# Performance work log

Hardware: AMD Instinct MI355X
Metric: run time of the kernel (lower is better)

Reference implementation:

```python
import jax, jax.numpy as jnp
import numpy as np

EMBED_DIM = 768
NUM_HEADS = 12
PROJ_DIM = EMBED_DIM // NUM_HEADS  # 64
M_FEATURES = 128
EPS = 1e-6


def _orthogonal_projection(key, m, d):
    # Faithful to create_projection_matrix(scaling=0): stacked transposed Q-factors
    # of iid gaussian blocks, rescaled by chi-distributed row norms.
    nb_full_blocks = m // d
    keys = jax.random.split(key, nb_full_blocks + 2)
    blocks = []
    for i in range(nb_full_blocks):
        q, _ = jnp.linalg.qr(jax.random.normal(keys[i], (d, d)))
        blocks.append(q.T)
    rem = m - nb_full_blocks * d
    if rem > 0:
        q, _ = jnp.linalg.qr(jax.random.normal(keys[nb_full_blocks], (d, d)))
        blocks.append(q.T[:rem])
    final = jnp.vstack(blocks)
    multiplier = jnp.linalg.norm(jax.random.normal(keys[-1], (m, d)), axis=1)
    return multiplier[:, None] * final


def setup_inputs() -> dict:
    key = jax.random.key(0)
    ks = jax.random.split(key, 8)
    B, L, E = 4, 4096, EMBED_DIM
    s = 1.0 / np.sqrt(E)
    inp = {
        "x": jax.random.normal(ks[0], (B, L, E), jnp.float32),
        "Wq": jax.random.normal(ks[1], (E, E), jnp.float32) * s,
        "bq": jnp.zeros((E,), jnp.float32),
        "Wk": jax.random.normal(ks[2], (E, E), jnp.float32) * s,
        "bk": jnp.zeros((E,), jnp.float32),
        "Wv": jax.random.normal(ks[3], (E, E), jnp.float32) * s,
        "bv": jnp.zeros((E,), jnp.float32),
        "Wo": jax.random.normal(ks[4], (E, E), jnp.float32) * s,
        "bo": jnp.zeros((E,), jnp.float32),
        "proj": _orthogonal_projection(ks[5], M_FEATURES, PROJ_DIM),
    }
    return inp


def _softmax_kernel(data, projection_matrix):
    # data: [B, L, H, D]; projection_matrix: [M, D]
    data_normalizer = 1.0 / jnp.sqrt(jnp.sqrt(jnp.float32(PROJ_DIM)))
    data = data_normalizer * data
    ratio = 1.0 / jnp.sqrt(jnp.float32(projection_matrix.shape[0]))
    data_dash = jnp.einsum("blhd,md->blhm", data, projection_matrix)
    diag_data = jnp.sum(jnp.square(data), axis=-1, keepdims=True) / 2.0  # [B,L,H,1]
    stab = jnp.max(data_dash, axis=-1, keepdims=True)
    return ratio * (jnp.exp(data_dash - diag_data - stab) + EPS)


def reference(x, Wq, bq, Wk, bk, Wv, bv, Wo, bo, proj):
    B, L, E = x.shape
    H, D = NUM_HEADS, PROJ_DIM

    def split_heads(t):
        return t.reshape(B, L, H, D)

    q = split_heads(x @ Wq + bq)
    k = split_heads(x @ Wk + bk)
    v = split_heads(x @ Wv + bv)

    q_prime = _softmax_kernel(q, proj)  # [B,L,H,M]
    k_prime = _softmax_kernel(k, proj)  # [B,L,H,M]

    # Linear-attention numerator/denominator (O(L) in sequence length).
    kvs = jnp.einsum("blhm,blhd->bhmd", k_prime, v)          # [B,H,M,D]
    num = jnp.einsum("blhm,bhmd->blhd", q_prime, kvs)        # [B,L,H,D]
    ks_sum = jnp.sum(k_prime, axis=1)                         # [B,H,M]
    den = jnp.einsum("blhm,bhm->blh", q_prime, ks_sum)        # [B,L,H]
    attention = num / den[..., None]                          # [B,L,H,D]

    # Faithful to source: transpose to [B,H,L,D] then reshape to [B,-1,E].
    concat = jnp.transpose(attention, (0, 2, 1, 3)).reshape(B, -1, E)
    return concat @ Wo + bo
```

## Files before the change

### kernel.cpp

```cpp
#include <hip/hip_runtime.h>

typedef _Float16 f16;
typedef __attribute__((ext_vector_type(8))) _Float16 half8;
typedef __attribute__((ext_vector_type(4))) _Float16 half4;
typedef __attribute__((ext_vector_type(4))) float f32x4;

#define DEVINL static __device__ __forceinline__

constexpr float NORMALIZER = 0.35355339059327373f;
constexpr float RATIO      = 0.08838834764831845f;
constexpr float FEPS       = 1e-6f;

constexpr size_t OFF_WQKVT = 0;
constexpr size_t OFF_WOT   = OFF_WQKVT + (size_t)2304*768*2;
constexpr size_t OFF_PROJF = OFF_WOT   + (size_t)768*768*2;
constexpr size_t OFF_KS    = OFF_PROJF + (size_t)128*64*2;
constexpr size_t OFF_KSP   = OFF_KS    + (size_t)48*128*4;
constexpr size_t OFF_KVST  = OFF_KSP   + (size_t)48*64*128*4;
constexpr size_t OFF_KVSP  = OFF_KVST  + (size_t)48*64*128*2;
constexpr size_t OFF_X16   = OFF_KVSP  + (size_t)16*48*128*64*4;
constexpr size_t OFF_ATT   = OFF_X16;
constexpr size_t OFF_Q16   = OFF_X16 + (size_t)16384*768*2;
constexpr size_t OFF_K16   = OFF_Q16 + (size_t)16384*768*2;
constexpr size_t OFF_VT    = OFF_K16 + (size_t)16384*768*2;
constexpr size_t OFF_KPT   = OFF_VT  + (size_t)16384*768*2;

DEVINL void gload_lds16(const f16* g, f16* lds) {
  __builtin_amdgcn_global_load_lds(
      (const __attribute__((address_space(1))) void*)g,
      (__attribute__((address_space(3))) void*)lds, 16, 0, 0);
}

#define VMCNT0    asm volatile("s_waitcnt vmcnt(0)" ::: "memory")
#define BAR       __builtin_amdgcn_s_barrier()

DEVINL void gemm256c(const f16* __restrict__ Ag, const f16* __restrict__ Bg,
                     f16* smem, f32x4 (&acc)[8][3], int w, int lane)
{
  constexpr int NT = 24;
  const int wm = w >> 2, wn = w & 3;
  const int c = lane & 15, g16 = lane >> 4;
  const int tid = threadIdx.x;

#pragma unroll
  for (int i = 0; i < 8; ++i)
#pragma unroll
    for (int j = 0; j < 3; ++j)
      acc[i][j] = f32x4{0.f, 0.f, 0.f, 0.f};

  auto SA = [&](int tt, f16* buf) {
#pragma unroll
    for (int u = 0; u < 2; ++u) {
      const int id = u * 512 + tid;
      const int r = id >> 2, sg = id & 3;
      const int seg = sg ^ ((r >> 1) & 3);
      gload_lds16(Ag + (size_t)r * 768 + tt * 32 + seg * 8, buf + (u * 512 + w * 64) * 8);
    }
  };
  auto SB = [&](int tt, f16* buf) {
    {
      const int r = tid >> 2, sg = tid & 3;
      const int seg = sg ^ ((r >> 1) & 3);
      gload_lds16(Bg + (size_t)r * 768 + tt * 32 + seg * 8, buf + 8192 + w * 64 * 8);
    }
    if (w < 4) {
      const int id = 512 + tid;
      const int r = id >> 2, sg = id & 3;
      const int seg = sg ^ ((r >> 1) & 3);
      gload_lds16(Bg + (size_t)r * 768 + tt * 32 + seg * 8, buf + 8192 + (512 + w * 64) * 8);
    }
  };
  auto RDA = [&](const f16* buf, int mh, half8 (&av)[4]) {
#pragma unroll
    for (int i = 0; i < 4; ++i) {
      const int r = wm * 128 + mh * 64 + i * 16 + c;
      av[i] = *(const half8*)(buf + r * 32 + ((g16 ^ ((r >> 1) & 3)) << 3));
    }
  };
  auto RDB = [&](const f16* buf, half8 (&bv)[3]) {
#pragma unroll
    for (int j = 0; j < 3; ++j) {
      const int r = wn * 48 + j * 16 + c;
      bv[j] = *(const half8*)(buf + 8192 + r * 32 + ((g16 ^ ((r >> 1) & 3)) << 3));
    }
  };

  SA(0, smem); SB(0, smem);
  VMCNT0;
  BAR;

#pragma unroll 1
  for (int t = 0; t < NT; ++t) {
    f16* bufR = smem + (t & 1) * 14336;
    f16* bufW = smem + ((t & 1) ^ 1) * 14336;
    const bool st = (t + 1) < NT;
    half8 av[4], bv[3];

    RDA(bufR, 0, av); RDB(bufR, bv);
    if (st) SA(t + 1, bufW);
    __builtin_amdgcn_s_setprio(1);
#pragma unroll
    for (int i = 0; i < 4; ++i)
#pragma unroll
      for (int j = 0; j < 3; ++j)
        acc[i][j] = __builtin_amdgcn_mfma_f32_16x16x32_f16(av[i], bv[j], acc[i][j], 0, 0, 0);
    __builtin_amdgcn_s_setprio(0);
    RDA(bufR, 1, av);
    if (st) SB(t + 1, bufW);
    __builtin_amdgcn_s_setprio(1);
#pragma unroll
    for (int i = 0; i < 4; ++i)
#pragma unroll
      for (int j = 0; j < 3; ++j)
        acc[4 + i][j] = __builtin_amdgcn_mfma_f32_16x16x32_f16(av[i], bv[j], acc[4 + i][j], 0, 0, 0);
    __builtin_amdgcn_s_setprio(0);
    VMCNT0;
    BAR;
  }
}

__global__ __launch_bounds__(512, 2) void k_gemm_qkv8(const f16* __restrict__ X16, const f16* __restrict__ WT,
    const float* __restrict__ bq, const float* __restrict__ bk, const float* __restrict__ bv,
    f16* __restrict__ Qo, f16* __restrict__ Ko, f16* __restrict__ VT)
{
  __shared__ f16 smem[28672];
  f32x4 acc[8][3];
  const int lin = blockIdx.x;
  const int xcd = lin & 7, chunk = lin >> 3;
  const int bx = xcd * 8 + chunk / 12;
  const int by = chunk % 12;
  const int brow0 = bx * 256;
  const int t = threadIdx.x, w = t >> 6, lane = t & 63;
  gemm256c(X16 + (size_t)brow0 * 768, WT + (size_t)by * 192 * 768, smem, acc, w, lane);

  const int wm = w >> 2, wn = w & 3;
  const int c = lane & 15, g16 = lane >> 4;
  const int which = by >> 2;
  const int colhdr = (by & 3) * 192;
  const float* bias = which == 0 ? bq : (which == 1 ? bk : bv);
  float bb[3];
#pragma unroll
  for (int j = 0; j < 3; ++j) bb[j] = bias[colhdr + wn * 48 + j * 16 + c];

  f16* ep = smem;
  if (which < 2) {
    f16* QK = which == 0 ? Qo : Ko;
#pragma unroll 1
    for (int p = 0; p < 2; ++p) {
      __syncthreads();
      if (wm == p) {
#pragma unroll
        for (int ii = 0; ii < 8; ++ii)
#pragma unroll
          for (int j = 0; j < 3; ++j)
#pragma unroll
            for (int r = 0; r < 4; ++r)
              ep[((ii >> 2) * 64 + (ii & 3) * 16 + g16 * 4 + r) * 200 + wn * 48 + j * 16 + c]
                  = (f16)(acc[ii][j][r] + bb[j]);
      }
      __syncthreads();
      const int row = t >> 2, sg = (t & 3) * 48;
      f16* dst = QK + (size_t)(brow0 + p * 128 + row) * 768 + colhdr + sg;
      const f16* sp = ep + row * 200 + sg;
#pragma unroll
      for (int u = 0; u < 6; ++u) *(half8*)(dst + u * 8) = *(const half8*)(sp + u * 8);
    }
  } else {
    const int bIdx = brow0 >> 12;
#pragma unroll 1
    for (int p = 0; p < 2; ++p) {
      __syncthreads();
      if (wm == p) {
#pragma unroll
        for (int ii = 0; ii < 8; ++ii)
#pragma unroll
          for (int j = 0; j < 3; ++j)
#pragma unroll
            for (int r = 0; r < 4; ++r)
              ep[(wn * 48 + j * 16 + c) * 136 + (ii >> 2) * 64 + (ii & 3) * 16 + g16 * 4 + r]
                  = (f16)(acc[ii][j][r] + bb[j]);
      }
      __syncthreads();
      if (t < 384) {
        const int cl = t >> 1, sg = (t & 1) * 64;
        const int vcol = colhdr + cl;
        const int h = vcol >> 6, d = vcol & 63;
        f16* dst = VT + ((size_t)(bIdx * 12 + h) * 64 + d) * 4096 + (brow0 & 4095) + p * 128 + sg;
        const f16* sp = ep + cl * 136 + sg;
#pragma unroll
        for (int u = 0; u < 8; ++u) *(half8*)(dst + u * 8) = *(const half8*)(sp + u * 8);
      }
    }
  }
}

__global__ __launch_bounds__(512, 2) void k_gemm_out8(const f16* __restrict__ ATT, const f16* __restrict__ WOT,
    const float* __restrict__ bo, float* __restrict__ out)
{
  __shared__ f16 smem[28672];
  f32x4 acc[8][3];
  const int lin = blockIdx.x;
  const int xcd = lin & 7, chunk = lin >> 3;
  const int bx = xcd * 8 + (chunk >> 2);
  const int by = chunk & 3;
  const int brow0 = bx * 256;
  const int t = threadIdx.x, w = t >> 6, lane = t & 63;
  gemm256c(ATT + (size_t)brow0 * 768, WOT + (size_t)by * 192 * 768, smem, acc, w, lane);

  const int wm = w >> 2, wn = w & 3;
  const int c = lane & 15, g16 = lane >> 4;
  float bb[3];
#pragma unroll
  for (int j = 0; j < 3; ++j) bb[j] = bo[by * 192 + wn * 48 + j * 16 + c];
#pragma unroll
  for (int ii = 0; ii < 8; ++ii) {
    const int row0 = brow0 + wm * 128 + (ii >> 2) * 64 + (ii & 3) * 16 + g16 * 4;
#pragma unroll
    for (int j = 0; j < 3; ++j) {
      const int col = by * 192 + wn * 48 + j * 16 + c;
#pragma unroll
      for (int r = 0; r < 4; ++r)
        out[(size_t)(row0 + r) * 768 + col] = acc[ii][j][r] + bb[j];
    }
  }
}

template<int BN>
DEVINL void gemm_tile(const f16* A, int lda, const f16* Bt, int ldb, int K,
                      f16* As, f16* Bs, f32x4 (&acc)[4][BN/32])
{
  constexpr int NF = BN/32;
  const int t = threadIdx.x;
  const int w = t >> 6, lane = t & 63;
  const int g = lane >> 4, c = lane & 15;
  const int wr = w >> 1, wc = w & 1;
  const int srow = lane >> 2;
  const int sseg = (lane & 3) * 8;

#pragma unroll
  for (int i = 0; i < 4; ++i)
#pragma unroll
    for (int j = 0; j < NF; ++j)
      acc[i][j] = f32x4{0.f, 0.f, 0.f, 0.f};

  for (int k0 = 0; k0 < K; k0 += 32) {
#pragma unroll
    for (int r = 0; r < 2; ++r) {
      const int rowblk = (w + 4*r) * 16;
      gload_lds16(A + (size_t)(rowblk + srow) * lda + k0 + sseg, As + rowblk*32);
    }
#pragma unroll
    for (int r = 0; r < BN/64; ++r) {
      const int rowblk = (w + 4*r) * 16;
      gload_lds16(Bt + (size_t)(rowblk + srow) * ldb + k0 + sseg, Bs + rowblk*32);
    }
    __syncthreads();
    half8 av[4], bv[NF];
#pragma unroll
    for (int i = 0; i < 4; ++i)
      av[i] = *(const half8*)(As + (wr*64 + i*16 + c)*32 + g*8);
#pragma unroll
    for (int j = 0; j < NF; ++j)
      bv[j] = *(const half8*)(Bs + (wc*(BN/2) + j*16 + c)*32 + g*8);
#pragma unroll
    for (int i = 0; i < 4; ++i)
#pragma unroll
      for (int j = 0; j < NF; ++j)
        acc[i][j] = __builtin_amdgcn_mfma_f32_16x16x32_f16(av[i], bv[j], acc[i][j], 0, 0, 0);
    __syncthreads();
  }
}

__global__ __launch_bounds__(256) void k_cast_x(const float* __restrict__ X, f16* __restrict__ X16)
{
  const size_t i = ((size_t)blockIdx.x*256 + threadIdx.x) * 4;
  const float4 v = *(const float4*)(X + i);
  half4 h;
  h[0] = (f16)v.x; h[1] = (f16)v.y; h[2] = (f16)v.z; h[3] = (f16)v.w;
  *(half4*)(X16 + i) = h;
}

__global__ __launch_bounds__(256) void k_transpose_w4(const float* __restrict__ Wq, const float* __restrict__ Wk,
    const float* __restrict__ Wv, const float* __restrict__ Wo, f16* __restrict__ WQKVT, f16* __restrict__ WOT)
{
  __shared__ float ls[64][65];
  const int t = threadIdx.x;
  const int k0 = blockIdx.x*64, n0 = blockIdx.y*64, z = blockIdx.z;
  const float* W = z == 0 ? Wq : (z == 1 ? Wk : (z == 2 ? Wv : Wo));
  f16* Wt = z < 3 ? (WQKVT + (size_t)z*768*768) : WOT;
#pragma unroll
  for (int it = 0; it < 4; ++it) {
    const int r = it*16 + (t >> 4);
    const int cs = (t & 15) * 4;
    const float4 v = *(const float4*)(W + (size_t)(k0 + r)*768 + n0 + cs);
    ls[r][cs+0] = v.x; ls[r][cs+1] = v.y; ls[r][cs+2] = v.z; ls[r][cs+3] = v.w;
  }
  __syncthreads();
  const int n = t >> 2;
  const int seg = (t & 3) * 16;
  half8 ov[2];
#pragma unroll
  for (int i = 0; i < 16; ++i) ov[i>>3][i&7] = (f16)ls[seg + i][n];
  f16* dst = Wt + (size_t)(n0 + n)*768 + k0 + seg;
  *(half8*)dst = ov[0];
  *(half8*)(dst + 8) = ov[1];
}

__global__ __launch_bounds__(256) void k_cast_proj(const float* __restrict__ P, f16* __restrict__ PF)
{
  const int i = blockIdx.x*256 + threadIdx.x;
  PF[i] = (f16)(NORMALIZER * P[i]);
}

DEVINL void feat_common(const f16* base, const f16* PROJF,
                        f16* qs, f16* ps, float* dd, float* diag_s)
{
  const int t = threadIdx.x, w = t >> 6, lane = t & 63;
#pragma unroll
  for (int it = 0; it < 2; ++it) {
    const int rowblk = it*32 + w*8;
    gload_lds16(base + (size_t)(rowblk + (lane>>3))*768 + (lane&7)*8, qs + rowblk*64);
  }
#pragma unroll
  for (int it = 0; it < 4; ++it) {
    const int rowblk = it*32 + w*8;
    gload_lds16(PROJF + (size_t)(rowblk + (lane>>3))*64 + (lane&7)*8, ps + rowblk*64);
  }
  __syncthreads();
  if (t < 64) {
    float s = 0.f;
    for (int d = 0; d < 64; ++d) { const float qv = (float)qs[t*64 + d]; s += qv*qv; }
    diag_s[t] = 0.0625f * s;
  }
  const int g = lane >> 4, c = lane & 15;
  const int wr = w >> 1, wc = w & 1;
  f32x4 facc[2][4];
#pragma unroll
  for (int i = 0; i < 2; ++i)
#pragma unroll
    for (int j = 0; j < 4; ++j) facc[i][j] = f32x4{0.f,0.f,0.f,0.f};
#pragma unroll
  for (int kk = 0; kk < 2; ++kk) {
    half8 av[2], bv[4];
#pragma unroll
    for (int i = 0; i < 2; ++i) av[i] = *(const half8*)(qs + (wr*32 + i*16 + c)*64 + kk*32 + g*8);
#pragma unroll
    for (int j = 0; j < 4; ++j) bv[j] = *(const half8*)(ps + (wc*64 + j*16 + c)*64 + kk*32 + g*8);
#pragma unroll
    for (int i = 0; i < 2; ++i)
#pragma unroll
      for (int j = 0; j < 4; ++j)
        facc[i][j] = __builtin_amdgcn_mfma_f32_16x16x32_f16(av[i], bv[j], facc[i][j], 0, 0, 0);
  }
#pragma unroll
  for (int i = 0; i < 2; ++i)
#pragma unroll
    for (int j = 0; j < 4; ++j)
#pragma unroll
      for (int r = 0; r < 4; ++r)
        dd[(wr*32 + i*16 + g*4 + r)*129 + wc*64 + j*16 + c] = facc[i][j][r];
  __syncthreads();
}

__global__ __launch_bounds__(256) void k_kfeat(const f16* __restrict__ Kin, const f16* __restrict__ PROJF,
    f16* __restrict__ KPT, float* __restrict__ KSP)
{
  __shared__ f16 qs[64*64];
  __shared__ f16 ps[128*64];
  __shared__ float dd[64*129];
  __shared__ float diag_s[64];
  const int t = threadIdx.x;
  const int lb = blockIdx.x, bh = blockIdx.y;
  const int b = bh / 12, h = bh - b*12;
  feat_common(Kin + ((size_t)(b*4096 + lb*64))*768 + h*64, PROJF, qs, ps, dd, diag_s);
  const int l = t >> 2, s = t & 3;
  float v[32];
#pragma unroll
  for (int j = 0; j < 32; ++j) v[j] = dd[l*129 + s*32 + j];
  float mx = v[0];
#pragma unroll
  for (int j = 1; j < 32; ++j) mx = fmaxf(mx, v[j]);
  mx = fmaxf(mx, __shfl_xor(mx, 1));
  mx = fmaxf(mx, __shfl_xor(mx, 2));
  const float off = diag_s[l] + mx;
#pragma unroll
  for (int j = 0; j < 32; ++j) dd[l*129 + s*32 + j] = RATIO * (__expf(v[j] - off) + FEPS);
  __syncthreads();
  if (t < 128) {
    float sm = 0.f;
    for (int l2 = 0; l2 < 64; ++l2) sm += dd[l2*129 + t];
    KSP[((size_t)bh*64 + lb)*128 + t] = sm;
  }
  const int m = t >> 1, hf = t & 1;
  half8 ov[4];
#pragma unroll
  for (int i2 = 0; i2 < 32; ++i2) ov[i2>>3][i2&7] = (f16)dd[(hf*32 + i2)*129 + m];
  f16* dst = KPT + ((size_t)bh*128 + m)*4096 + lb*64 + hf*32;
#pragma unroll
  for (int q8 = 0; q8 < 4; ++q8) *(half8*)(dst + q8*8) = ov[q8];
}

__global__ __launch_bounds__(256) void k_kvs(const f16* __restrict__ KPT, const f16* __restrict__ VT,
    float* __restrict__ KVSP)
{
  __shared__ f16 As[128*32], Bs[64*32];
  f32x4 acc[4][2];
  const int chunk = blockIdx.x, bh = blockIdx.y;
  gemm_tile<64>(KPT + (size_t)bh*128*4096 + chunk*256, 4096,
                VT  + (size_t)bh*64*4096  + chunk*256, 4096, 256, As, Bs, acc);
  const int t = threadIdx.x, w = t>>6, lane = t&63, g = lane>>4, c = lane&15;
  const int wr = w>>1, wc = w&1;
  float* dst = KVSP + (size_t)(chunk*48 + bh)*128*64;
#pragma unroll
  for (int i = 0; i < 4; ++i) {
    const int row0 = wr*64 + i*16 + g*4;
#pragma unroll
    for (int j = 0; j < 2; ++j) {
      const int col = wc*32 + j*16 + c;
#pragma unroll
      for (int r = 0; r < 4; ++r) dst[(size_t)(row0 + r)*64 + col] = acc[i][j][r];
    }
  }
}

__global__ __launch_bounds__(256) void k_reduce(const float* __restrict__ KVSP, const float* __restrict__ KSP,
    f16* __restrict__ KVST, float* __restrict__ KS)
{
  const int i = blockIdx.x*256 + threadIdx.x;
  if (i < 48*128*64) {
    const int bh = i >> 13, md = i & 8191, m = md >> 6, d = md & 63;
    float s = 0.f;
#pragma unroll
    for (int c = 0; c < 16; ++c) s += KVSP[((size_t)(c*48 + bh)*128 + m)*64 + d];
    KVST[((size_t)bh*64 + d)*128 + m] = (f16)s;
  }
  if (i < 48*128) {
    const int bh = i >> 7, m = i & 127;
    float s = 0.f;
#pragma unroll 8
    for (int lb = 0; lb < 64; ++lb) s += KSP[((size_t)bh*64 + lb)*128 + m];
    KS[i] = s;
  }
}

__global__ __launch_bounds__(256) void k_qfn(const f16* __restrict__ Q, const f16* __restrict__ PROJF,
    const float* __restrict__ KS, const f16* __restrict__ KVST, f16* __restrict__ ATT)
{
  __shared__ f16 qs[64*64];
  __shared__ f16 ps[128*64];
  __shared__ float dd[64*129];
  __shared__ float diag_s[64];
  __shared__ float den_s[64];
  __shared__ f16 qp[64*128];
  __shared__ float ks_s[128];
  const int t = threadIdx.x;
  const int lb = blockIdx.x, bh = blockIdx.y;
  const int b = bh / 12, h = bh - b*12;
  if (t < 128) ks_s[t] = KS[bh*128 + t];
  feat_common(Q + ((size_t)(b*4096 + lb*64))*768 + h*64, PROJF, qs, ps, dd, diag_s);

  const int w = t >> 6, lane = t & 63, g16 = lane >> 4, c = lane & 15;
  const int wr = w >> 1, wc = w & 1;
  half8 bv2[2][4];
#pragma unroll
  for (int j = 0; j < 2; ++j) {
    const int d = wc*32 + j*16 + c;
#pragma unroll
    for (int kk = 0; kk < 4; ++kk)
      bv2[j][kk] = *(const half8*)(KVST + (size_t)bh*8192 + d*128 + kk*32 + g16*8);
  }

  const int l = t >> 2, s = t & 3;
  float v[32];
#pragma unroll
  for (int j = 0; j < 32; ++j) v[j] = dd[l*129 + s*32 + j];
  float mx = v[0];
#pragma unroll
  for (int j = 1; j < 32; ++j) mx = fmaxf(mx, v[j]);
  mx = fmaxf(mx, __shfl_xor(mx, 1));
  mx = fmaxf(mx, __shfl_xor(mx, 2));
  const float off = diag_s[l] + mx;
  half8 ov[4];
  float dp = 0.f;
#pragma unroll
  for (int j = 0; j < 32; ++j) {
    const float e = RATIO * (__expf(v[j] - off) + FEPS);
    ov[j>>3][j&7] = (f16)e;
    dp += e * ks_s[s*32 + j];
  }
  dp += __shfl_xor(dp, 1);
  dp += __shfl_xor(dp, 2);
  if (s == 0) den_s[l] = dp;
#pragma unroll
  for (int k = 0; k < 4; ++k)
    *(half8*)(qp + l*128 + (((4*s + k) ^ (l & 7)) << 3)) = ov[k];
  __syncthreads();

  f32x4 acc2[2][2];
#pragma unroll
  for (int i = 0; i < 2; ++i)
#pragma unroll
    for (int j = 0; j < 2; ++j) acc2[i][j] = f32x4{0.f,0.f,0.f,0.f};
#pragma unroll
  for (int kk = 0; kk < 4; ++kk) {
    half8 av2[2];
#pragma unroll
    for (int i = 0; i < 2; ++i) {
      const int l2 = wr*32 + i*16 + c;
      av2[i] = *(const half8*)(qp + l2*128 + (((kk*4 + g16) ^ (l2 & 7)) << 3));
    }
#pragma unroll
    for (int i = 0; i < 2; ++i)
#pragma unroll
      for (int j = 0; j < 2; ++j)
        acc2[i][j] = __builtin_amdgcn_mfma_f32_16x16x32_f16(av2[i], bv2[j][kk], acc2[i][j], 0, 0, 0);
  }

  f16* ep = ps;
#pragma unroll
  for (int i = 0; i < 2; ++i)
#pragma unroll
    for (int j = 0; j < 2; ++j)
#pragma unroll
      for (int r = 0; r < 4; ++r) {
        const int l3 = wr*32 + i*16 + g16*4 + r;
        ep[l3*72 + wc*32 + j*16 + c] = (f16)(acc2[i][j][r] / den_s[l3]);
      }
  __syncthreads();
  const int row = t >> 2, sg = (t & 3) * 16;
  f16* dst = ATT + ((size_t)bh*4096 + lb*64 + row)*64 + sg;
  const f16* sp = ep + row*72 + sg;
  *(half8*)dst = *(const half8*)sp;
  *(half8*)(dst + 8) = *(const half8*)(sp + 8);
}

extern "C" void kernel_launch(void* const* d_in, const int* in_sizes, int n_in,
                              void* d_out, int out_size, void* d_ws, size_t ws_size,
                              hipStream_t stream)
{
  const float* x    = (const float*)d_in[0];
  const float* Wq   = (const float*)d_in[1];
  const float* bq   = (const float*)d_in[2];
  const float* Wk   = (const float*)d_in[3];
  const float* bk   = (const float*)d_in[4];
  const float* Wv   = (const float*)d_in[5];
  const float* bv   = (const float*)d_in[6];
  const float* Wo   = (const float*)d_in[7];
  const float* bo   = (const float*)d_in[8];
  const float* proj = (const float*)d_in[9];
  float* out = (float*)d_out;
  char* ws = (char*)d_ws;

  f16*   WQKVT = (f16*)(ws + OFF_WQKVT);
  f16*   WOT   = (f16*)(ws + OFF_WOT);
  f16*   PROJF = (f16*)(ws + OFF_PROJF);
  float* KS    = (float*)(ws + OFF_KS);
  float* KSP   = (float*)(ws + OFF_KSP);
  f16*   KVST  = (f16*)(ws + OFF_KVST);
  float* KVSP  = (float*)(ws + OFF_KVSP);
  f16*   X16   = (f16*)(ws + OFF_X16);
  f16*   ATT   = (f16*)(ws + OFF_ATT);
  f16*   Q16   = (f16*)(ws + OFF_Q16);
  f16*   K16   = (f16*)(ws + OFF_K16);
  f16*   VT    = (f16*)(ws + OFF_VT);
  f16*   KPT   = (f16*)(ws + OFF_KPT);

  k_cast_x<<<12288, 256, 0, stream>>>(x, X16);
  k_transpose_w4<<<dim3(12,12,4), 256, 0, stream>>>(Wq, Wk, Wv, Wo, WQKVT, WOT);
  k_cast_proj<<<32, 256, 0, stream>>>(proj, PROJF);

  k_gemm_qkv8<<<768, 512, 0, stream>>>(X16, WQKVT, bq, bk, bv, Q16, K16, VT);
  k_kfeat<<<dim3(64,48), 256, 0, stream>>>(K16, PROJF, KPT, KSP);
  k_kvs<<<dim3(16,48), 256, 0, stream>>>(KPT, VT, KVSP);
  k_reduce<<<1536, 256, 0, stream>>>(KVSP, KSP, KVST, KS);
  k_qfn<<<dim3(64,48), 256, 0, stream>>>(Q16, PROJF, KS, KVST, ATT);
  k_gemm_out8<<<256, 512, 0, stream>>>(ATT, WOT, bo, out);
}
```

Measured before the change: 257.2 us.

## Fuse prep kernels, parallelize row reductions, and halve kvs split chunks

Merges the x cast, weight transposes and projection cast into one launch to cut launch overhead. In the feature kernels, the diagonal-norm and column-sum reductions are spread across all threads with shuffles instead of running on a subset with long serial loops. The kvs split-K count drops from 16 to 8 chunks, so each block does more work and the reduce step reads half as many partials. The trade-off is fewer blocks for kvs, which may leave the GPU underused.

```diff
diff --git a/kernel.cpp b/kernel.cpp
--- a/kernel.cpp
+++ b/kernel.cpp
@@ -18,7 +18,7 @@
 constexpr size_t OFF_KSP   = OFF_KS    + (size_t)48*128*4;
 constexpr size_t OFF_KVST  = OFF_KSP   + (size_t)48*64*128*4;
 constexpr size_t OFF_KVSP  = OFF_KVST  + (size_t)48*64*128*2;
-constexpr size_t OFF_X16   = OFF_KVSP  + (size_t)16*48*128*64*4;
+constexpr size_t OFF_X16   = OFF_KVSP  + (size_t)8*48*128*64*4;
 constexpr size_t OFF_ATT   = OFF_X16;
 constexpr size_t OFF_Q16   = OFF_X16 + (size_t)16384*768*2;
 constexpr size_t OFF_K16   = OFF_Q16 + (size_t)16384*768*2;
@@ -271,21 +271,27 @@
   }
 }
 
-__global__ __launch_bounds__(256) void k_cast_x(const float* __restrict__ X, f16* __restrict__ X16)
-{
-  const size_t i = ((size_t)blockIdx.x*256 + threadIdx.x) * 4;
-  const float4 v = *(const float4*)(X + i);
-  half4 h;
-  h[0] = (f16)v.x; h[1] = (f16)v.y; h[2] = (f16)v.z; h[3] = (f16)v.w;
-  *(half4*)(X16 + i) = h;
-}
-
-__global__ __launch_bounds__(256) void k_transpose_w4(const float* __restrict__ Wq, const float* __restrict__ Wk,
-    const float* __restrict__ Wv, const float* __restrict__ Wo, f16* __restrict__ WQKVT, f16* __restrict__ WOT)
+__global__ __launch_bounds__(256) void k_prep(const float* __restrict__ X, f16* __restrict__ X16,
+    const float* __restrict__ P, f16* __restrict__ PF,
+    const float* __restrict__ Wq, const float* __restrict__ Wk,
+    const float* __restrict__ Wv, const float* __restrict__ Wo,
+    f16* __restrict__ WQKVT, f16* __restrict__ WOT)
 {
   __shared__ float ls[64][65];
   const int t = threadIdx.x;
-  const int k0 = blockIdx.x*64, n0 = blockIdx.y*64, z = blockIdx.z;
+  if (blockIdx.x < 12288) {
+    const size_t i = ((size_t)blockIdx.x*256 + t) * 4;
+    const float4 v = *(const float4*)(X + i);
+    half4 h;
+    h[0] = (f16)v.x; h[1] = (f16)v.y; h[2] = (f16)v.z; h[3] = (f16)v.w;
+    *(half4*)(X16 + i) = h;
+    if (blockIdx.x == 0)
+      for (int i2 = t; i2 < 8192; i2 += 256) PF[i2] = (f16)(NORMALIZER * P[i2]);
+    return;
+  }
+  const int zz = blockIdx.x - 12288;
+  const int z = zz / 144, rem = zz - z*144;
+  const int k0 = (rem / 12) * 64, n0 = (rem % 12) * 64;
   const float* W = z == 0 ? Wq : (z == 1 ? Wk : (z == 2 ? Wv : Wo));
   f16* Wt = z < 3 ? (WQKVT + (size_t)z*768*768) : WOT;
 #pragma unroll
@@ -306,12 +312,6 @@
   *(half8*)(dst + 8) = ov[1];
 }
 
-__global__ __launch_bounds__(256) void k_cast_proj(const float* __restrict__ P, f16* __restrict__ PF)
-{
-  const int i = blockIdx.x*256 + threadIdx.x;
-  PF[i] = (f16)(NORMALIZER * P[i]);
-}
-
 DEVINL void feat_common(const f16* base, const f16* PROJF,
                         f16* qs, f16* ps, float* dd, float* diag_s)
 {
@@ -327,10 +327,19 @@
     gload_lds16(PROJF + (size_t)(rowblk + (lane>>3))*64 + (lane&7)*8, ps + rowblk*64);
   }
   __syncthreads();
-  if (t < 64) {
+  {
+    const int row = t >> 2, q = t & 3;
+    const f16* kr = qs + row*64 + q*16;
+    half8 v0 = *(const half8*)(kr);
+    half8 v1 = *(const half8*)(kr + 8);
     float s = 0.f;
-    for (int d = 0; d < 64; ++d) { const float qv = (float)qs[t*64 + d]; s += qv*qv; }
-    diag_s[t] = 0.0625f * s;
+#pragma unroll
+    for (int d2 = 0; d2 < 8; ++d2) { float a = (float)v0[d2]; s += a*a; }
+#pragma unroll
+    for (int d2 = 0; d2 < 8; ++d2) { float a = (float)v1[d2]; s += a*a; }
+    s += __shfl_xor(s, 1);
+    s += __shfl_xor(s, 2);
+    if (q == 0) diag_s[row] = 0.0625f * s;
   }
   const int g = lane >> 4, c = lane & 15;
   const int wr = w >> 1, wc = w & 1;
@@ -386,10 +395,13 @@
 #pragma unroll
   for (int j = 0; j < 32; ++j) dd[l*129 + s*32 + j] = RATIO * (__expf(v[j] - off) + FEPS);
   __syncthreads();
-  if (t < 128) {
+  {
+    const int m = t >> 1, hf = t & 1;
     float sm = 0.f;
-    for (int l2 = 0; l2 < 64; ++l2) sm += dd[l2*129 + t];
-    KSP[((size_t)bh*64 + lb)*128 + t] = sm;
+#pragma unroll 8
+    for (int l2 = hf*32; l2 < hf*32 + 32; ++l2) sm += dd[l2*129 + m];
+    sm += __shfl_xor(sm, 1);
+    if (hf == 0) KSP[((size_t)bh*64 + lb)*128 + m] = sm;
   }
   const int m = t >> 1, hf = t & 1;
   half8 ov[4];
@@ -406,8 +418,8 @@
   __shared__ f16 As[128*32], Bs[64*32];
   f32x4 acc[4][2];
   const int chunk = blockIdx.x, bh = blockIdx.y;
-  gemm_tile<64>(KPT + (size_t)bh*128*4096 + chunk*256, 4096,
-                VT  + (size_t)bh*64*4096  + chunk*256, 4096, 256, As, Bs, acc);
+  gemm_tile<64>(KPT + (size_t)bh*128*4096 + chunk*512, 4096,
+                VT  + (size_t)bh*64*4096  + chunk*512, 4096, 512, As, Bs, acc);
   const int t = threadIdx.x, w = t>>6, lane = t&63, g = lane>>4, c = lane&15;
   const int wr = w>>1, wc = w&1;
   float* dst = KVSP + (size_t)(chunk*48 + bh)*128*64;
@@ -431,7 +443,7 @@
     const int bh = i >> 13, md = i & 8191, m = md >> 6, d = md & 63;
     float s = 0.f;
 #pragma unroll
-    for (int c = 0; c < 16; ++c) s += KVSP[((size_t)(c*48 + bh)*128 + m)*64 + d];
+    for (int c = 0; c < 8; ++c) s += KVSP[((size_t)(c*48 + bh)*128 + m)*64 + d];
     KVST[((size_t)bh*64 + d)*128 + m] = (f16)s;
   }
   if (i < 48*128) {
@@ -565,13 +577,10 @@
   f16*   VT    = (f16*)(ws + OFF_VT);
   f16*   KPT   = (f16*)(ws + OFF_KPT);
 
-  k_cast_x<<<12288, 256, 0, stream>>>(x, X16);
-  k_transpose_w4<<<dim3(12,12,4), 256, 0, stream>>>(Wq, Wk, Wv, Wo, WQKVT, WOT);
-  k_cast_proj<<<32, 256, 0, stream>>>(proj, PROJF);
-
+  k_prep<<<12864, 256, 0, stream>>>(x, X16, proj, PROJF, Wq, Wk, Wv, Wo, WQKVT, WOT);
   k_gemm_qkv8<<<768, 512, 0, stream>>>(X16, WQKVT, bq, bk, bv, Q16, K16, VT);
   k_kfeat<<<dim3(64,48), 256, 0, stream>>>(K16, PROJF, KPT, KSP);
-  k_kvs<<<dim3(16,48), 256, 0, stream>>>(KPT, VT, KVSP);
+  k_kvs<<<dim3(8,48), 256, 0, stream>>>(KPT, VT, KVSP);
   k_reduce<<<1536, 256, 0, stream>>>(KVSP, KSP, KVST, KS);
   k_qfn<<<dim3(64,48), 256, 0, stream>>>(Q16, PROJF, KS, KVST, ATT);
   k_gemm_out8<<<256, 512, 0, stream>>>(ATT, WOT, bo, out);
```

Result: faster. 246.1 us (-4.3%).
